# Kernel optimization log

Measured on AMD Instinct MI355X. Metric: run time of the kernel, lower is better.

## Reference

```python
import jax, jax.numpy as jnp
import numpy as np

NOT_EPSILON = 1.0

def swishmax(x, axis):
    # x * exp(x - max) normalized by sum(|.|) + 1 over `axis`
    xexp = x * jnp.exp(x - jnp.max(x, axis=axis, keepdims=True))
    return xexp / (jnp.sum(jnp.abs(xexp), axis=axis, keepdims=True) + NOT_EPSILON)

def setup_inputs() -> dict:
    key = jax.random.key(0)
    ks = jax.random.split(key, 8)
    B, S, D = 2, 512, 256
    std = 0.02
    x = jax.random.normal(ks[0], (B, S, D), dtype=jnp.float32)
    w_pre = jax.random.normal(ks[1], (D, D), dtype=jnp.float32) * std
    w_q   = jax.random.normal(ks[2], (D, D), dtype=jnp.float32) * std
    w_k   = jax.random.normal(ks[3], (D, D), dtype=jnp.float32) * std
    w_va  = jax.random.normal(ks[4], (D, D), dtype=jnp.float32) * std
    w_al  = jax.random.normal(ks[5], (D, D), dtype=jnp.float32) * std
    w_vo  = jax.random.normal(ks[6], (D, D), dtype=jnp.float32) * std
    w_end = jax.random.normal(ks[7], (D, D), dtype=jnp.float32) * std
    return {"x": x, "w_pre": w_pre, "w_q": w_q, "w_k": w_k,
            "w_va": w_va, "w_al": w_al, "w_vo": w_vo, "w_end": w_end}

def reference(x, w_pre, w_q, w_k, w_va, w_al, w_vo, w_end):
    # pre: module_1d = Linear(D, D, bias=False)
    X = x @ w_pre.T                                    # [B,S,D]
    # FractalAttention depth=2 (base case): row_dims=(-3,)
    q = X + X @ w_q.T                                  # residual query proj
    k = X + X @ w_k.T                                  # residual key proj
    # batchify: key lhs -> [B,Sk,1,D], query rhs -> [B,1,Sq,D]
    raw = k[:, :, None, :] * q[:, None, :, :]          # [B,Sk,Sq,D]
    logits = raw + raw @ w_al.T                        # residual logit proj over D
    scale = swishmax(logits, axis=-3)                  # normalize over Sk
    v = X + X @ w_va.T
    vs = v[:, :, None, :] * scale                      # [B,Sk,Sq,D]
    vsum = jnp.sum(vs, axis=-3)                        # [B,Sq,D]
    vout = vsum + vsum @ w_vo.T
    X = X + vout                                       # transformer residual
    X = X @ w_end.T                                    # end: module_1d
    return X
```

## Files before the change

kernel.cpp:

```cpp
#include <hip/hip_runtime.h>
#include <hip/hip_bf16.h>


typedef __attribute__((ext_vector_type(8))) short short8;
typedef __attribute__((ext_vector_type(4))) float f32x4;
typedef __attribute__((ext_vector_type(8))) _Float16 half8;
typedef __attribute__((ext_vector_type(4))) _Float16 half4;

#define DD 256
#define SS 512
#define LOG2E 1.4426950408889634f
#define LN2   0.6931471805599453f

__device__ __forceinline__ unsigned short f2bf(float f) {
  unsigned int b = __float_as_uint(f);
  b += 0x7FFFu + ((b >> 16) & 1u);
  return (unsigned short)(b >> 16);
}
__device__ __forceinline__ short8 cvt8(f32x4 lo, f32x4 hi) {
  short8 r;
  r[0]=(short)f2bf(lo[0]); r[1]=(short)f2bf(lo[1]);
  r[2]=(short)f2bf(lo[2]); r[3]=(short)f2bf(lo[3]);
  r[4]=(short)f2bf(hi[0]); r[5]=(short)f2bf(hi[1]);
  r[6]=(short)f2bf(hi[2]); r[7]=(short)f2bf(hi[3]);
  return r;
}
__device__ __forceinline__ void gload16(const void* g, void* l) {
  __builtin_amdgcn_global_load_lds(
      (const __attribute__((address_space(1))) void*)g,
      (__attribute__((address_space(3))) void*)l,
      16, 0, 0);
}

__global__ __launch_bounds__(256) void prep_weights(
    const float* __restrict__ w0, const float* __restrict__ w1,
    const float* __restrict__ w2, const float* __restrict__ w3,
    const float* __restrict__ w4, const float* __restrict__ w5,
    const float* __restrict__ wal, unsigned short* __restrict__ out)
{
  const int bi = blockIdx.x;
  const int m = bi >> 5;
  const int off = ((bi & 31) * 256 + threadIdx.x) * 8;
  const float* src = m==0?w0: m==1?w1: m==2?w2: m==3?w3: m==4?w4: m==5?w5: wal;
  f32x4 a = *(const f32x4*)(src + off);
  f32x4 b = *(const f32x4*)(src + off + 4);
  if (m == 6) {
    const int e = off >> 8, d = off & 255;
#pragma unroll
    for (int jj = 0; jj < 4; ++jj) {
      if (e == d + jj)     a[jj] += 1.0f;
      if (e == d + 4 + jj) b[jj] += 1.0f;
    }
    half8 h;
#pragma unroll
    for (int jj = 0; jj < 4; ++jj) {
      h[jj]     = (_Float16)a[jj];
      h[jj + 4] = (_Float16)b[jj];
    }
    *(half8*)(out + (size_t)m * 65536 + off) = h;
  } else {
    *(short8*)(out + (size_t)m * 65536 + off) = cvt8(a, b);
  }
}

__global__ __launch_bounds__(256) void linear_bf(
    const float* __restrict__ A, const unsigned short* __restrict__ Wbf,
    const float* __restrict__ res1, const float* __restrict__ res2,
    float* __restrict__ out)
{
  const int bi = blockIdx.x;
  const int rb = (bi >> 2) * 16;
  const int cb = (bi & 3) * 64;
  const int tid = threadIdx.x;
  const int wv = tid >> 6, lane = tid & 63;
  const int g = lane >> 4, c = lane & 15;
  const int arow = rb + c;
  const int wrow = cb + wv * 16 + c;

  f32x4 acc = (f32x4){0.f, 0.f, 0.f, 0.f};
#pragma unroll
  for (int ks = 0; ks < 8; ++ks) {
    const int d0 = ks * 32 + g * 8;
    f32x4 a0 = *(const f32x4*)(A + arow * DD + d0);
    f32x4 a1 = *(const f32x4*)(A + arow * DD + d0 + 4);
    short8 av = cvt8(a0, a1);
    short8 bv = *(const short8*)(Wbf + wrow * DD + d0);
    acc = __builtin_amdgcn_mfma_f32_16x16x32_bf16(av, bv, acc, 0, 0, 0);
  }
#pragma unroll
  for (int j = 0; j < 4; ++j) {
    const int ro = rb + g * 4 + j;
    const int co = cb + wv * 16 + c;
    float v = acc[j];
    if (res1) v += res1[ro * DD + co];
    if (res2) v += res2[ro * DD + co];
    out[ro * DD + co] = v;
  }
}

__global__ __launch_bounds__(256) void linear_qkv(
    const float* __restrict__ X,
    const unsigned short* __restrict__ Wq, const unsigned short* __restrict__ Wk,
    const unsigned short* __restrict__ Wv,
    _Float16* __restrict__ qout,
    _Float16* __restrict__ kfrag, _Float16* __restrict__ vfrag)
{
  __shared__ _Float16 kl[16][64];
  __shared__ _Float16 vl[16][64];

  const int bi = blockIdx.x;
  const int rb = (bi >> 2) * 16;
  const int cb = (bi & 3) * 64;
  const int tid = threadIdx.x;
  const int wv = tid >> 6, lane = tid & 63;
  const int g = lane >> 4, c = lane & 15;
  const int arow = rb + c;
  const int wrow = cb + wv * 16 + c;

  f32x4 aq = (f32x4){0.f,0.f,0.f,0.f};
  f32x4 ak = (f32x4){0.f,0.f,0.f,0.f};
  f32x4 av_ = (f32x4){0.f,0.f,0.f,0.f};
#pragma unroll
  for (int ks = 0; ks < 8; ++ks) {
    const int d0 = ks * 32 + g * 8;
    f32x4 a0 = *(const f32x4*)(X + arow * DD + d0);
    f32x4 a1 = *(const f32x4*)(X + arow * DD + d0 + 4);
    short8 af = cvt8(a0, a1);
    short8 bq = *(const short8*)(Wq + wrow * DD + d0);
    aq = __builtin_amdgcn_mfma_f32_16x16x32_bf16(af, bq, aq, 0, 0, 0);
    short8 bk = *(const short8*)(Wk + wrow * DD + d0);
    ak = __builtin_amdgcn_mfma_f32_16x16x32_bf16(af, bk, ak, 0, 0, 0);
    short8 bv = *(const short8*)(Wv + wrow * DD + d0);
    av_ = __builtin_amdgcn_mfma_f32_16x16x32_bf16(af, bv, av_, 0, 0, 0);
  }
#pragma unroll
  for (int j = 0; j < 4; ++j) {
    const int ro = rb + g * 4 + j;
    const int co = cb + wv * 16 + c;
    const float base = X[ro * DD + co];
    qout[ro * DD + co] = (_Float16)((base + aq[j]) * LOG2E);
    kl[g * 4 + j][wv * 16 + c] = (_Float16)(base + ak[j]);
    vl[g * 4 + j][wv * 16 + c] = (_Float16)(base + av_[j]);
  }
  __syncthreads();

  const int b  = rb >> 9;
  const int t2 = (rb >> 4) & 31;
  const int cg = cb >> 5;

  if (tid < 128) {
    const int ksl = tid >> 6, lane2 = tid & 63;
    const int g2 = lane2 >> 4, c2 = lane2 & 15;
    half8 h = *(const half8*)&kl[c2][ksl * 32 + g2 * 8];
    *(half8*)(kfrag + (size_t)b * 131072 + (size_t)t2 * 4096
              + (cg + ksl) * 512 + lane2 * 8) = h;
  }
  {
    const int sl = tid >> 7, il = (tid >> 6) & 1, lane2 = tid & 63;
    const int g2 = lane2 >> 4, c2 = lane2 & 15;
    half4 h = *(const half4*)&vl[c2][sl * 32 + il * 16 + g2 * 4];
    *(half4*)(vfrag + (size_t)b * 131072 + (size_t)t2 * 4096
              + (cg + sl) * 512 + il * 256 + lane2 * 4) = h;
  }
}

__global__ __launch_bounds__(256, 3) void fractal_attn(
    const _Float16* __restrict__ walI,
    const _Float16* __restrict__ qf,
    const _Float16* __restrict__ kfrag,
    const _Float16* __restrict__ vfrag,
    float* __restrict__ vsum)
{
  __shared__ _Float16 kt[2][4096];

  const int bid = blockIdx.x;
  const int eh = bid & 1;
  const int sq = (bid >> 1) & 511;
  const int b  = bid >> 10;
  const int tid = threadIdx.x;
  const int wv = tid >> 6;
  const int lane = tid & 63;
  const int g = lane >> 4, c = lane & 15;
  const int slice = eh * 4 + wv;
  const int sbase = slice * 32;

  const _Float16* ktile0 = kfrag + (size_t)b * 131072;
  auto stage = [&](int t) {
    const _Float16* src = ktile0 + (size_t)t * 4096;
    _Float16* dst = &kt[t & 1][0];
    gload16(src + tid * 8,        dst + tid * 8);
    gload16(src + 2048 + tid * 8, dst + 2048 + tid * 8);
  };

  stage(0);

  half8 afrag[2][8];
  {
    const _Float16* qrow = qf + (size_t)(b * SS + sq) * DD;
    half8 q8[8];
#pragma unroll
    for (int ks = 0; ks < 8; ++ks)
      q8[ks] = *(const half8*)(qrow + ks * 32 + g * 8);
#pragma unroll
    for (int i = 0; i < 2; ++i) {
      const int e = sbase + i * 16 + c;
      const _Float16* wrow = walI + (size_t)e * DD;
#pragma unroll
      for (int ks = 0; ks < 8; ++ks)
        afrag[i][ks] = (*(const half8*)(wrow + ks * 32 + g * 8)) * q8[ks];
    }
  }

  const _Float16* vfb = vfrag + (size_t)b * 131072 + slice * 512 + lane * 4;

  float mst[8], sst[8], vst[8];
#pragma unroll
  for (int s = 0; s < 8; ++s) { mst[s] = -1e30f; sst[s] = 0.f; vst[s] = 0.f; }

  half8 bf[8];
  half4 vqA[2], vqB[2];
  f32x4 accA[2], accB[2];
  const f32x4 zeroc = (f32x4){0.f, 0.f, 0.f, 0.f};

#define DSREAD(BUF)                                                 \
  {                                                                 \
    const _Float16* kb_ = &kt[BUF][0];                              \
    _Pragma("unroll")                                               \
    for (int ks = 0; ks < 8; ++ks)                                  \
      bf[ks] = *(const half8*)(kb_ + ks * 512 + lane * 8);          \
  }
#define LOADV(T2, VQ)                                               \
  {                                                                 \
    const _Float16* vf_ = vfb + (size_t)(T2) * 4096;                \
    VQ[0] = *(const half4*)(vf_);                                   \
    VQ[1] = *(const half4*)(vf_ + 256);                             \
  }
#define MFMA_INTO(ACC)                                              \
  {                                                                 \
    __builtin_amdgcn_s_setprio(1);                                  \
    ACC[0] = __builtin_amdgcn_mfma_f32_16x16x32_f16(                \
        afrag[0][0], bf[0], zeroc, 0, 0, 0);                        \
    ACC[1] = __builtin_amdgcn_mfma_f32_16x16x32_f16(                \
        afrag[1][0], bf[0], zeroc, 0, 0, 0);                        \
    _Pragma("unroll")                                               \
    for (int ks = 1; ks < 8; ++ks) {                                \
      ACC[0] = __builtin_amdgcn_mfma_f32_16x16x32_f16(              \
          afrag[0][ks], bf[ks], ACC[0], 0, 0, 0);                   \
      ACC[1] = __builtin_amdgcn_mfma_f32_16x16x32_f16(              \
          afrag[1][ks], bf[ks], ACC[1], 0, 0, 0);                   \
    }                                                               \
    __builtin_amdgcn_s_setprio(0);                                  \
  }
#define UPDATE(ACC, VQ)                                             \
  {                                                                 \
    _Pragma("unroll")                                               \
    for (int i = 0; i < 2; ++i)                                     \
      _Pragma("unroll")                                             \
      for (int j = 0; j < 4; ++j) {                                 \
        const int s = i * 4 + j;                                    \
        const float L = ACC[i][j];                                  \
        mst[s] = fmaxf(mst[s], L);                                  \
        const float p = L * __builtin_amdgcn_exp2f(L);              \
        sst[s] += fabsf(p);                                         \
        vst[s] = fmaf((float)VQ[i][j], p, vst[s]);                  \
      }                                                             \
  }

  LOADV(0, vqA);
  __syncthreads();
  DSREAD(0);
  stage(1);
  MFMA_INTO(accA);

#pragma unroll 1
  for (int t = 1; t < 31; t += 2) {
    __syncthreads();
    DSREAD(t & 1);
    LOADV(t, vqB);
    stage(t + 1);
    MFMA_INTO(accB);
    UPDATE(accA, vqA);

    __syncthreads();
    DSREAD((t + 1) & 1);
    LOADV(t + 1, vqA);
    if (t + 2 < 32) stage(t + 2);
    MFMA_INTO(accA);
    UPDATE(accB, vqB);
  }

  __syncthreads();
  DSREAD(1);
  LOADV(31, vqB);
  MFMA_INTO(accB);
  UPDATE(accA, vqA);
  UPDATE(accB, vqB);

#undef DSREAD
#undef LOADV
#undef MFMA_INTO
#undef UPDATE

#pragma unroll
  for (int mask = 1; mask <= 8; mask <<= 1) {
#pragma unroll
    for (int s = 0; s < 8; ++s) {
      mst[s] = fmaxf(mst[s], __shfl_xor(mst[s], mask));
      sst[s] += __shfl_xor(sst[s], mask);
      vst[s] += __shfl_xor(vst[s], mask);
    }
  }

  if (c == 0) {
    float* orow = vsum + (size_t)(b * SS + sq) * DD;
#pragma unroll
    for (int i = 0; i < 2; ++i) {
      f32x4 o;
#pragma unroll
      for (int j = 0; j < 4; ++j) {
        const int s = i * 4 + j;
        const float tt = LN2 * __builtin_amdgcn_exp2f(-mst[s]);
        o[j] = vst[s] * tt / (sst[s] * tt + 1.0f);
      }
      *(f32x4*)(orow + sbase + i * 16 + g * 4) = o;
    }
  }
}

extern "C" void kernel_launch(void* const* d_in, const int* in_sizes, int n_in,
                              void* d_out, int out_size, void* d_ws, size_t ws_size,
                              hipStream_t stream) {
  const float* x     = (const float*)d_in[0];
  const float* w_pre = (const float*)d_in[1];
  const float* w_q   = (const float*)d_in[2];
  const float* w_k   = (const float*)d_in[3];
  const float* w_va  = (const float*)d_in[4];
  const float* w_al  = (const float*)d_in[5];
  const float* w_vo  = (const float*)d_in[6];
  const float* w_end = (const float*)d_in[7];
  float* out = (float*)d_out;

  char* ws = (char*)d_ws;
  float*    X     = (float*)(ws);
  float*    Y     = (float*)(ws + (1 << 20));
  float*    vsum  = (float*)(ws + (2 << 20));
  _Float16* qf16  = (_Float16*)(ws + (3 << 20));
  _Float16* kfrag = (_Float16*)(ws + (3 << 20) + (512 << 10));
  _Float16* vfrag = (_Float16*)(ws + (4 << 20));
  unsigned short* wbf = (unsigned short*)(ws + (4 << 20) + (512 << 10));

  prep_weights<<<224, 256, 0, stream>>>(w_pre, w_q, w_k, w_va, w_vo, w_end,
                                        w_al, wbf);
  linear_bf<<<256, 256, 0, stream>>>(x, wbf + 0 * 65536, nullptr, nullptr, X);
  linear_qkv<<<256, 256, 0, stream>>>(X, wbf + 1 * 65536, wbf + 2 * 65536,
                                      wbf + 3 * 65536, qf16, kfrag, vfrag);
  fractal_attn<<<2048, 256, 0, stream>>>((const _Float16*)(wbf + 6 * 65536),
                                         qf16, kfrag, vfrag, vsum);
  linear_bf<<<256, 256, 0, stream>>>(vsum, wbf + 4 * 65536, vsum, X, Y);
  linear_bf<<<256, 256, 0, stream>>>(Y, wbf + 5 * 65536, nullptr, nullptr, out);
}
```

Before: 118.1 us.

## Fuse weight prep with pre-projection and keep V in fp32

Merges the weight conversion kernel and the first linear layer into one launch. Extra blocks compute X = x @ w_pre^T directly from fp32 weights, converting to bf16 on the fly. This removes one kernel launch and the serial dependency between the two. V fragments are now stored and loaded as fp32 instead of fp16, which doubles V traffic in the attention kernel but removes the per-element conversion and improves accuracy.

```diff
diff --git a/kernel.cpp b/kernel.cpp
--- a/kernel.cpp
+++ b/kernel.cpp
@@ -32,35 +32,64 @@
       16, 0, 0);
 }
 
-__global__ __launch_bounds__(256) void prep_weights(
-    const float* __restrict__ w0, const float* __restrict__ w1,
-    const float* __restrict__ w2, const float* __restrict__ w3,
-    const float* __restrict__ w4, const float* __restrict__ w5,
-    const float* __restrict__ wal, unsigned short* __restrict__ out)
+__global__ __launch_bounds__(256) void prep_and_X(
+    const float* __restrict__ x,  const float* __restrict__ w_pre,
+    const float* __restrict__ w1, const float* __restrict__ w2,
+    const float* __restrict__ w3, const float* __restrict__ w4,
+    const float* __restrict__ w5, const float* __restrict__ wal,
+    unsigned short* __restrict__ wbf, float* __restrict__ X)
 {
   const int bi = blockIdx.x;
-  const int m = bi >> 5;
-  const int off = ((bi & 31) * 256 + threadIdx.x) * 8;
-  const float* src = m==0?w0: m==1?w1: m==2?w2: m==3?w3: m==4?w4: m==5?w5: wal;
-  f32x4 a = *(const f32x4*)(src + off);
-  f32x4 b = *(const f32x4*)(src + off + 4);
-  if (m == 6) {
-    const int e = off >> 8, d = off & 255;
-#pragma unroll
-    for (int jj = 0; jj < 4; ++jj) {
-      if (e == d + jj)     a[jj] += 1.0f;
-      if (e == d + 4 + jj) b[jj] += 1.0f;
+  const int tid = threadIdx.x;
+  if (bi < 192) {
+    const int m = 1 + (bi >> 5);
+    const int off = ((bi & 31) * 256 + tid) * 8;
+    const float* src = m==1?w1: m==2?w2: m==3?w3: m==4?w4: m==5?w5: wal;
+    f32x4 a = *(const f32x4*)(src + off);
+    f32x4 b = *(const f32x4*)(src + off + 4);
+    if (m == 6) {
+      const int e = off >> 8, d = off & 255;
+#pragma unroll
+      for (int jj = 0; jj < 4; ++jj) {
+        if (e == d + jj)     a[jj] += 1.0f;
+        if (e == d + 4 + jj) b[jj] += 1.0f;
+      }
+      half8 h;
+#pragma unroll
+      for (int jj = 0; jj < 4; ++jj) {
+        h[jj]     = (_Float16)a[jj];
+        h[jj + 4] = (_Float16)b[jj];
+      }
+      *(half8*)(wbf + (size_t)m * 65536 + off) = h;
+    } else {
+      *(short8*)(wbf + (size_t)m * 65536 + off) = cvt8(a, b);
     }
-    half8 h;
-#pragma unroll
-    for (int jj = 0; jj < 4; ++jj) {
-      h[jj]     = (_Float16)a[jj];
-      h[jj + 4] = (_Float16)b[jj];
-    }
-    *(half8*)(out + (size_t)m * 65536 + off) = h;
-  } else {
-    *(short8*)(out + (size_t)m * 65536 + off) = cvt8(a, b);
-  }
+    return;
+  }
+
+  const int bi2 = bi - 192;
+  const int rb = (bi2 >> 2) * 16;
+  const int cb = (bi2 & 3) * 64;
+  const int wv = tid >> 6, lane = tid & 63;
+  const int g = lane >> 4, c = lane & 15;
+  const int arow = rb + c;
+  const int wrow = cb + wv * 16 + c;
+
+  f32x4 acc = (f32x4){0.f, 0.f, 0.f, 0.f};
+#pragma unroll
+  for (int ks = 0; ks < 8; ++ks) {
+    const int d0 = ks * 32 + g * 8;
+    f32x4 a0 = *(const f32x4*)(x + arow * DD + d0);
+    f32x4 a1 = *(const f32x4*)(x + arow * DD + d0 + 4);
+    short8 av = cvt8(a0, a1);
+    f32x4 b0 = *(const f32x4*)(w_pre + wrow * DD + d0);
+    f32x4 b1 = *(const f32x4*)(w_pre + wrow * DD + d0 + 4);
+    short8 bv = cvt8(b0, b1);
+    acc = __builtin_amdgcn_mfma_f32_16x16x32_bf16(av, bv, acc, 0, 0, 0);
+  }
+#pragma unroll
+  for (int j = 0; j < 4; ++j)
+    X[(rb + g * 4 + j) * DD + cb + wv * 16 + c] = acc[j];
 }
 
 __global__ __launch_bounds__(256) void linear_bf(
@@ -103,10 +132,10 @@
     const unsigned short* __restrict__ Wq, const unsigned short* __restrict__ Wk,
     const unsigned short* __restrict__ Wv,
     _Float16* __restrict__ qout,
-    _Float16* __restrict__ kfrag, _Float16* __restrict__ vfrag)
+    _Float16* __restrict__ kfrag, float* __restrict__ vfrag)
 {
   __shared__ _Float16 kl[16][64];
-  __shared__ _Float16 vl[16][64];
+  __shared__ float    vl[16][64];
 
   const int bi = blockIdx.x;
   const int rb = (bi >> 2) * 16;
@@ -140,7 +169,7 @@
     const float base = X[ro * DD + co];
     qout[ro * DD + co] = (_Float16)((base + aq[j]) * LOG2E);
     kl[g * 4 + j][wv * 16 + c] = (_Float16)(base + ak[j]);
-    vl[g * 4 + j][wv * 16 + c] = (_Float16)(base + av_[j]);
+    vl[g * 4 + j][wv * 16 + c] = base + av_[j];
   }
   __syncthreads();
 
@@ -158,8 +187,8 @@
   {
     const int sl = tid >> 7, il = (tid >> 6) & 1, lane2 = tid & 63;
     const int g2 = lane2 >> 4, c2 = lane2 & 15;
-    half4 h = *(const half4*)&vl[c2][sl * 32 + il * 16 + g2 * 4];
-    *(half4*)(vfrag + (size_t)b * 131072 + (size_t)t2 * 4096
+    f32x4 h = *(const f32x4*)&vl[c2][sl * 32 + il * 16 + g2 * 4];
+    *(f32x4*)(vfrag + (size_t)b * 131072 + (size_t)t2 * 4096
               + (cg + sl) * 512 + il * 256 + lane2 * 4) = h;
   }
 }
@@ -168,7 +197,7 @@
     const _Float16* __restrict__ walI,
     const _Float16* __restrict__ qf,
     const _Float16* __restrict__ kfrag,
-    const _Float16* __restrict__ vfrag,
+    const float* __restrict__ vfrag,
     float* __restrict__ vsum)
 {
   __shared__ _Float16 kt[2][4096];
@@ -211,14 +240,14 @@
     }
   }
 
-  const _Float16* vfb = vfrag + (size_t)b * 131072 + slice * 512 + lane * 4;
+  const float* vfb = vfrag + (size_t)b * 131072 + slice * 512 + lane * 4;
 
   float mst[8], sst[8], vst[8];
 #pragma unroll
   for (int s = 0; s < 8; ++s) { mst[s] = -1e30f; sst[s] = 0.f; vst[s] = 0.f; }
 
   half8 bf[8];
-  half4 vqA[2], vqB[2];
+  f32x4 vqA[2], vqB[2];
   f32x4 accA[2], accB[2];
   const f32x4 zeroc = (f32x4){0.f, 0.f, 0.f, 0.f};
 
@@ -231,9 +260,9 @@
   }
 #define LOADV(T2, VQ)                                               \
   {                                                                 \
-    const _Float16* vf_ = vfb + (size_t)(T2) * 4096;                \
-    VQ[0] = *(const half4*)(vf_);                                   \
-    VQ[1] = *(const half4*)(vf_ + 256);                             \
+    const float* vf_ = vfb + (size_t)(T2) * 4096;                   \
+    VQ[0] = *(const f32x4*)(vf_);                                   \
+    VQ[1] = *(const f32x4*)(vf_ + 256);                             \
   }
 #define MFMA_INTO(ACC)                                              \
   {                                                                 \
@@ -262,7 +291,7 @@
         mst[s] = fmaxf(mst[s], L);                                  \
         const float p = L * __builtin_amdgcn_exp2f(L);              \
         sst[s] += fabsf(p);                                         \
-        vst[s] = fmaf((float)VQ[i][j], p, vst[s]);                  \
+        vst[s] = fmaf(VQ[i][j], p, vst[s]);                         \
       }                                                             \
   }
 
@@ -346,12 +375,11 @@
   float*    vsum  = (float*)(ws + (2 << 20));
   _Float16* qf16  = (_Float16*)(ws + (3 << 20));
   _Float16* kfrag = (_Float16*)(ws + (3 << 20) + (512 << 10));
-  _Float16* vfrag = (_Float16*)(ws + (4 << 20));
-  unsigned short* wbf = (unsigned short*)(ws + (4 << 20) + (512 << 10));
-
-  prep_weights<<<224, 256, 0, stream>>>(w_pre, w_q, w_k, w_va, w_vo, w_end,
-                                        w_al, wbf);
-  linear_bf<<<256, 256, 0, stream>>>(x, wbf + 0 * 65536, nullptr, nullptr, X);
+  float*    vfrag = (float*)(ws + (4 << 20));
+  unsigned short* wbf = (unsigned short*)(ws + (5 << 20));
+
+  prep_and_X<<<448, 256, 0, stream>>>(x, w_pre, w_q, w_k, w_va, w_vo, w_end,
+                                      w_al, wbf, X);
   linear_qkv<<<256, 256, 0, stream>>>(X, wbf + 1 * 65536, wbf + 2 * 65536,
                                       wbf + 3 * 65536, qf16, kfrag, vfrag);
   fractal_attn<<<2048, 256, 0, stream>>>((const _Float16*)(wbf + 6 * 65536),
```

New measurement: 241.8 us. 105% more time.
